# Performance work log

Measured on AMD Instinct MI355X. Metric: run time of the kernel, lower is better.

Reference implementation:

```python
import jax, jax.numpy as jnp
import numpy as np

T, B, D, H, O = 512, 256, 512, 256, 256
MLP_DIMS = [(D, 100), (100, 100), (100, 100), (100, 50), (50, H)]


def _linear_init(key, fan_in, fan_out):
    kw, kb = jax.random.split(key)
    lim = 1.0 / np.sqrt(fan_in)
    w = jax.random.uniform(kw, (fan_out, fan_in), minval=-lim, maxval=lim, dtype=jnp.float32)
    b = jax.random.uniform(kb, (fan_out,), minval=-lim, maxval=lim, dtype=jnp.float32)
    return w, b


def setup_inputs() -> dict:
    key = jax.random.key(0)
    ks = jax.random.split(key, 8)
    inp = {"x": jax.random.normal(ks[0], (T, B, D), dtype=jnp.float32)}
    for i, (fi, fo) in enumerate(MLP_DIMS):
        w, b = _linear_init(ks[1 + i], fi, fo)
        inp[f"wm{i + 1}"] = w
        inp[f"bm{i + 1}"] = b
    inp["wx"], inp["bx"] = _linear_init(ks[6], D, H)
    inp["wo"], inp["bo"] = _linear_init(ks[7], H, O)
    return inp


def reference(x, wm1, bm1, wm2, bm2, wm3, bm3, wm4, bm4, wm5, bm5, wx, bx, wo, bo):
    def step(h, xt):
        # xt: [B, D], h: [B, H]
        lx = xt @ wx.T + bx                      # linearX
        a = jax.nn.relu(xt @ wm1.T + bm1)        # layerMLP chain
        a = jax.nn.relu(a @ wm2.T + bm2)
        a = jax.nn.relu(a @ wm3.T + bm3)
        a = jax.nn.relu(a @ wm4.T + bm4)
        fx = jax.nn.sigmoid(a @ wm5.T + bm5)
        gate = fx * jax.nn.sigmoid(lx)
        h_new = jax.nn.relu(jnp.roll(h, 1, axis=-1) + gate)
        return h_new, None

    h0 = jnp.zeros((x.shape[1], wx.shape[0]), dtype=x.dtype)
    hidden, _ = jax.lax.scan(step, h0, x)
    output = hidden @ wo.T + bo                  # h2o
    return output, hidden
```

## Files before the change

kernel.cpp:

```cpp
#include <hip/hip_runtime.h>

typedef __attribute__((ext_vector_type(8))) short short8;
typedef __attribute__((ext_vector_type(4))) float f32x4;

#define OFF_WX 0
#define OFF_W1 131072
#define OFF_W2 196608
#define OFF_W3 212992
#define OFF_W4 229376
#define OFF_W5 237568
#define W_TOTAL 253952
#define TR 32

static __device__ __forceinline__ unsigned short f2bf(float f) {
    unsigned int u = __builtin_bit_cast(unsigned int, f);
    unsigned int r = (u + 0x7fffu + ((u >> 16) & 1u)) >> 16;
    return (unsigned short)r;
}
static __device__ __forceinline__ float bf2f(unsigned short h) {
    unsigned int u = ((unsigned int)h) << 16;
    return __builtin_bit_cast(float, u);
}
static __device__ __forceinline__ float sigmoidf(float z) {
    return 1.f / (1.f + __expf(-z));
}
static __device__ __forceinline__ void stA(unsigned short* dst, int r, int c, float v) {
    dst[(r << 7) + (((c >> 3) ^ (r & 7)) << 3) + (c & 7)] = f2bf(v);
}

__global__ __launch_bounds__(256) void prep_kernel(
    const float* __restrict__ wx, const float* __restrict__ wm1,
    const float* __restrict__ wm2, const float* __restrict__ wm3,
    const float* __restrict__ wm4, const float* __restrict__ wm5,
    unsigned short* __restrict__ wb, float* __restrict__ hid)
{
    const int stride = gridDim.x * blockDim.x;
    for (int idx = blockIdx.x * blockDim.x + threadIdx.x; idx < W_TOTAL; idx += stride) {
        float v;
        if (idx < OFF_W1) {
            v = wx[idx];
        } else if (idx < OFF_W2) {
            int j = idx - OFF_W1; int n = j >> 9, k = j & 511;
            v = (n < 100) ? wm1[n * 512 + k] : 0.f;
        } else if (idx < OFF_W3) {
            int j = idx - OFF_W2; int n = j >> 7, k = j & 127;
            v = (n < 100 && k < 100) ? wm2[n * 100 + k] : 0.f;
        } else if (idx < OFF_W4) {
            int j = idx - OFF_W3; int n = j >> 7, k = j & 127;
            v = (n < 100 && k < 100) ? wm3[n * 100 + k] : 0.f;
        } else if (idx < OFF_W5) {
            int j = idx - OFF_W4; int n = j >> 7, k = j & 127;
            v = (n < 50 && k < 100) ? wm4[n * 100 + k] : 0.f;
        } else {
            int j = idx - OFF_W5; int n = j >> 6, k = j & 63;
            v = (k < 50) ? wm5[n * 50 + k] : 0.f;
        }
        wb[idx] = f2bf(v);
    }
    for (int idx = blockIdx.x * blockDim.x + threadIdx.x; idx < 65536; idx += stride)
        hid[idx] = 0.f;
}

template<int KLOOP, int NI, typename Epi>
static __device__ __forceinline__ void stageS(const unsigned short* As,
                                              const unsigned short* __restrict__ Wg,
                                              int wave, int lane, Epi&& epi)
{
    f32x4 acc[NI][2];
#pragma unroll
    for (int i = 0; i < NI; i++) { acc[i][0] = {0,0,0,0}; acc[i][1] = {0,0,0,0}; }
    const int kp  = (lane >> 4) << 3;
    const int l15 = lane & 15;
#pragma unroll
    for (int k0 = 0; k0 < KLOOP; k0 += 32) {
        const int kb = (k0 >> 3) + (lane >> 4);
        short8 af[2];
#pragma unroll
        for (int mt = 0; mt < 2; mt++) {
            const int rm = mt * 16 + l15;
            af[mt] = *(const short8*)(As + (rm << 7) + ((kb ^ (rm & 7)) << 3));
        }
#pragma unroll
        for (int i = 0; i < NI; i++) {
            const int nt = wave + (i << 2);
            short8 bf = *(const short8*)(Wg + (nt * 16 + l15) * KLOOP + k0 + kp);
#pragma unroll
            for (int mt = 0; mt < 2; mt++)
                acc[i][mt] = __builtin_amdgcn_mfma_f32_16x16x32_bf16(
                    af[mt], bf, acc[i][mt], 0, 0, 0);
        }
    }
#pragma unroll
    for (int i = 0; i < NI; i++)
#pragma unroll
        for (int mt = 0; mt < 2; mt++)
            epi(i, wave + (i << 2), mt, acc[i][mt]);
}

__global__ __launch_bounds__(256, 4) void srnn_main(
    const float* __restrict__ x,
    const float* __restrict__ b1, const float* __restrict__ b2,
    const float* __restrict__ b3, const float* __restrict__ b4,
    const float* __restrict__ b5, const float* __restrict__ bx,
    const unsigned short* __restrict__ wb, float* __restrict__ hid)
{
    __shared__ __align__(16) unsigned short Xs[TR * 512];
    __shared__ __align__(16) unsigned short A1[TR * 128];
    unsigned short* A2 = Xs;
    unsigned short* Gs = Xs + 4096;

    const int tid  = threadIdx.x;
    const int wave = tid >> 6, lane = tid & 63;
    const int blk  = blockIdx.x;
    const int b    = blk >> 4;
    const int t0   = (blk & 15) << 5;
    const int l15  = lane & 15;
    const int rb   = (lane >> 4) << 2;
    const int kp   = (lane >> 4) << 3;

    {
        const int m0 = tid >> 7, c4 = tid & 127;
        const float* xbase = x + ((size_t)(t0 + m0) * 256 + b) * 512 + (c4 << 2);
        float4 xr[16];
#pragma unroll
        for (int it = 0; it < 16; it++)
            xr[it] = *(const float4*)(xbase + (size_t)it * 262144);
        const int blk8 = c4 >> 1, halfoff = (c4 & 1) << 2;
#pragma unroll
        for (int it = 0; it < 16; it++) {
            const int m = m0 + 2 * it;
            unsigned int p0 = (unsigned int)f2bf(xr[it].x) | ((unsigned int)f2bf(xr[it].y) << 16);
            unsigned int p1 = (unsigned int)f2bf(xr[it].z) | ((unsigned int)f2bf(xr[it].w) << 16);
            *(uint2*)&Xs[(m << 9) + ((blk8 ^ (m & 7)) << 3) + halfoff] = make_uint2(p0, p1);
        }
    }
    __syncthreads();

    f32x4 am1[2][2], alx[4][2];
#pragma unroll
    for (int i = 0; i < 2; i++) { am1[i][0] = {0,0,0,0}; am1[i][1] = {0,0,0,0}; }
#pragma unroll
    for (int i = 0; i < 4; i++) { alx[i][0] = {0,0,0,0}; alx[i][1] = {0,0,0,0}; }
    {
        const unsigned short* W1 = wb + OFF_W1;
        const unsigned short* WX = wb + OFF_WX;
#pragma unroll 4
        for (int k0 = 0; k0 < 512; k0 += 32) {
            const int kb = (k0 >> 3) + (lane >> 4);
            short8 af[2];
#pragma unroll
            for (int mt = 0; mt < 2; mt++) {
                const int rm = mt * 16 + l15;
                af[mt] = *(const short8*)(Xs + (rm << 9) + ((kb ^ (rm & 7)) << 3));
            }
#pragma unroll
            for (int i = 0; i < 2; i++) {
                short8 bf = *(const short8*)(W1 + ((wave + (i << 2)) * 16 + l15) * 512 + k0 + kp);
                am1[i][0] = __builtin_amdgcn_mfma_f32_16x16x32_bf16(af[0], bf, am1[i][0], 0, 0, 0);
                am1[i][1] = __builtin_amdgcn_mfma_f32_16x16x32_bf16(af[1], bf, am1[i][1], 0, 0, 0);
            }
#pragma unroll
            for (int i = 0; i < 4; i++) {
                short8 bf = *(const short8*)(WX + ((wave + (i << 2)) * 16 + l15) * 512 + k0 + kp);
                alx[i][0] = __builtin_amdgcn_mfma_f32_16x16x32_bf16(af[0], bf, alx[i][0], 0, 0, 0);
                alx[i][1] = __builtin_amdgcn_mfma_f32_16x16x32_bf16(af[1], bf, alx[i][1], 0, 0, 0);
            }
        }
#pragma unroll
        for (int i = 0; i < 2; i++) {
            const int c = (wave + (i << 2)) * 16 + l15;
            const float bb = (c < 100) ? b1[c] : 0.f;
#pragma unroll
            for (int mt = 0; mt < 2; mt++)
#pragma unroll
                for (int q = 0; q < 4; q++)
                    stA(A1, mt * 16 + rb + q, c,
                        (c < 100) ? fmaxf(am1[i][mt][q] + bb, 0.f) : 0.f);
        }
    }
    __syncthreads();

    stageS<128, 2>(A1, wb + OFF_W2, wave, lane, [&](int, int nt, int mt, f32x4 v) {
        const int c = nt * 16 + l15;
        const float bb = (c < 100) ? b2[c] : 0.f;
#pragma unroll
        for (int q = 0; q < 4; q++)
            stA(A2, mt * 16 + rb + q, c, (c < 100) ? fmaxf(v[q] + bb, 0.f) : 0.f);
    });
    __syncthreads();

    stageS<128, 2>(A2, wb + OFF_W3, wave, lane, [&](int, int nt, int mt, f32x4 v) {
        const int c = nt * 16 + l15;
        const float bb = (c < 100) ? b3[c] : 0.f;
#pragma unroll
        for (int q = 0; q < 4; q++)
            stA(A1, mt * 16 + rb + q, c, (c < 100) ? fmaxf(v[q] + bb, 0.f) : 0.f);
    });
    __syncthreads();

    stageS<128, 1>(A1, wb + OFF_W4, wave, lane, [&](int, int nt, int mt, f32x4 v) {
        const int c = nt * 16 + l15;
        const float bb = (c < 50) ? b4[c] : 0.f;
#pragma unroll
        for (int q = 0; q < 4; q++)
            stA(A2, mt * 16 + rb + q, c, (c < 50) ? fmaxf(v[q] + bb, 0.f) : 0.f);
    });
    __syncthreads();

    stageS<64, 4>(A2, wb + OFF_W5, wave, lane, [&](int i, int nt, int mt, f32x4 v) {
        const int c = nt * 16 + l15;
        const float bb5 = b5[c], bbx = bx[c];
#pragma unroll
        for (int q = 0; q < 4; q++) {
            const float g = sigmoidf(v[q] + bb5) * sigmoidf(alx[i][mt][q] + bbx);
            Gs[(mt * 16 + rb + q) * 256 + c] = f2bf(g);
        }
    });
    __syncthreads();

    {
        const int j = tid;
        const int base = (j + t0 + 1) & 255;
        float ph = 0.f;
#pragma unroll
        for (int m = 0; m < TR; m++)
            ph += bf2f(Gs[(m << 8) + ((base + m) & 255)]);
        atomicAdd(hid + b * 256 + j, ph);
    }
}

__global__ __launch_bounds__(256) void out_kernel(
    const float* __restrict__ hid, const float* __restrict__ wo,
    const float* __restrict__ bo, float* __restrict__ out)
{
    __shared__ __align__(16) float hrow[256];
    const int b = blockIdx.x, o = threadIdx.x;
    float h = hid[b * 256 + o];
    hrow[o] = h;
    out[65536 + b * 256 + o] = h;
    __syncthreads();
    const float4* wrow = (const float4*)(wo + o * 256);
    float s = bo[o];
#pragma unroll 8
    for (int k4 = 0; k4 < 64; k4++) {
        float4 w = wrow[k4];
        float4 hh = *(const float4*)&hrow[k4 * 4];
        s += hh.x * w.x + hh.y * w.y + hh.z * w.z + hh.w * w.w;
    }
    out[b * 256 + o] = s;
}

extern "C" void kernel_launch(void* const* d_in, const int* in_sizes, int n_in,
                              void* d_out, int out_size, void* d_ws, size_t ws_size,
                              hipStream_t stream)
{
    (void)in_sizes; (void)n_in; (void)out_size; (void)ws_size;
    const float* x   = (const float*)d_in[0];
    const float* wm1 = (const float*)d_in[1];
    const float* bm1 = (const float*)d_in[2];
    const float* wm2 = (const float*)d_in[3];
    const float* bm2 = (const float*)d_in[4];
    const float* wm3 = (const float*)d_in[5];
    const float* bm3 = (const float*)d_in[6];
    const float* wm4 = (const float*)d_in[7];
    const float* bm4 = (const float*)d_in[8];
    const float* wm5 = (const float*)d_in[9];
    const float* bm5 = (const float*)d_in[10];
    const float* wx  = (const float*)d_in[11];
    const float* bx  = (const float*)d_in[12];
    const float* wo  = (const float*)d_in[13];
    const float* bo  = (const float*)d_in[14];
    float* out = (float*)d_out;

    unsigned short* wb = (unsigned short*)d_ws;
    float* hid = (float*)((char*)d_ws + (size_t)W_TOTAL * 2);

    prep_kernel<<<512, 256, 0, stream>>>(wx, wm1, wm2, wm3, wm4, wm5, wb, hid);
    srnn_main<<<4096, 256, 0, stream>>>(x, bm1, bm2, bm3, bm4, bm5, bx, wb, hid);
    out_kernel<<<256, 256, 0, stream>>>(hid, wo, bo, out);
}
```

Before: 611.1 us.

## Use 512-thread blocks with per-wave N-tile split, wider swizzle, fused sigmoid gate

Doubles the main kernel's block size to 8 waves so that each wave owns fewer output tiles per stage. Stage 4 splits work across N and M tiles to keep all waves busy. The LDS XOR swizzle is widened from 8 to 16 row groups, and the gate buffer is also swizzled, to cut bank conflicts. The two sigmoids are fused into one reciprocal of a product of exponentials. This raises per-block parallelism and lowers register pressure, at the cost of more threads contending for the same shared memory and barriers.

Result: slower. 626.3 us (+2.5%).

```diff
diff --git a/kernel.cpp b/kernel.cpp
--- a/kernel.cpp
+++ b/kernel.cpp
@@ -21,12 +21,15 @@
     unsigned int u = ((unsigned int)h) << 16;
     return __builtin_bit_cast(float, u);
 }
-static __device__ __forceinline__ float sigmoidf(float z) {
-    return 1.f / (1.f + __expf(-z));
+static __device__ __forceinline__ float gate2(float a, float b) {
+    float ea = __expf(-a), eb = __expf(-b);
+    return __builtin_amdgcn_rcpf((1.f + ea) * (1.f + eb));
 }
 static __device__ __forceinline__ void stA(unsigned short* dst, int r, int c, float v) {
-    dst[(r << 7) + (((c >> 3) ^ (r & 7)) << 3) + (c & 7)] = f2bf(v);
-}
+    dst[(r << 7) + (((c >> 3) ^ (r & 15)) << 3) + (c & 7)] = f2bf(v);
+}
+
+#define MFMA(a, bfr, acc) __builtin_amdgcn_mfma_f32_16x16x32_bf16((a), (bfr), (acc), 0, 0, 0)
 
 __global__ __launch_bounds__(256) void prep_kernel(
     const float* __restrict__ wx, const float* __restrict__ wm1,
@@ -61,43 +64,7 @@
         hid[idx] = 0.f;
 }
 
-template<int KLOOP, int NI, typename Epi>
-static __device__ __forceinline__ void stageS(const unsigned short* As,
-                                              const unsigned short* __restrict__ Wg,
-                                              int wave, int lane, Epi&& epi)
-{
-    f32x4 acc[NI][2];
-#pragma unroll
-    for (int i = 0; i < NI; i++) { acc[i][0] = {0,0,0,0}; acc[i][1] = {0,0,0,0}; }
-    const int kp  = (lane >> 4) << 3;
-    const int l15 = lane & 15;
-#pragma unroll
-    for (int k0 = 0; k0 < KLOOP; k0 += 32) {
-        const int kb = (k0 >> 3) + (lane >> 4);
-        short8 af[2];
-#pragma unroll
-        for (int mt = 0; mt < 2; mt++) {
-            const int rm = mt * 16 + l15;
-            af[mt] = *(const short8*)(As + (rm << 7) + ((kb ^ (rm & 7)) << 3));
-        }
-#pragma unroll
-        for (int i = 0; i < NI; i++) {
-            const int nt = wave + (i << 2);
-            short8 bf = *(const short8*)(Wg + (nt * 16 + l15) * KLOOP + k0 + kp);
-#pragma unroll
-            for (int mt = 0; mt < 2; mt++)
-                acc[i][mt] = __builtin_amdgcn_mfma_f32_16x16x32_bf16(
-                    af[mt], bf, acc[i][mt], 0, 0, 0);
-        }
-    }
-#pragma unroll
-    for (int i = 0; i < NI; i++)
-#pragma unroll
-        for (int mt = 0; mt < 2; mt++)
-            epi(i, wave + (i << 2), mt, acc[i][mt]);
-}
-
-__global__ __launch_bounds__(256, 4) void srnn_main(
+__global__ __launch_bounds__(512, 8) void srnn_main(
     const float* __restrict__ x,
     const float* __restrict__ b1, const float* __restrict__ b2,
     const float* __restrict__ b3, const float* __restrict__ b4,
@@ -110,7 +77,7 @@
     unsigned short* Gs = Xs + 4096;
 
     const int tid  = threadIdx.x;
-    const int wave = tid >> 6, lane = tid & 63;
+    const int w    = tid >> 6, lane = tid & 63;
     const int blk  = blockIdx.x;
     const int b    = blk >> 4;
     const int t0   = (blk & 15) << 5;
@@ -119,112 +86,156 @@
     const int kp   = (lane >> 4) << 3;
 
     {
-        const int m0 = tid >> 7, c4 = tid & 127;
+        const int m0 = tid >> 7;
+        const int c4 = tid & 127;
         const float* xbase = x + ((size_t)(t0 + m0) * 256 + b) * 512 + (c4 << 2);
-        float4 xr[16];
-#pragma unroll
-        for (int it = 0; it < 16; it++)
-            xr[it] = *(const float4*)(xbase + (size_t)it * 262144);
+        float4 xr[8];
+#pragma unroll
+        for (int it = 0; it < 8; it++)
+            xr[it] = *(const float4*)(xbase + (size_t)it * 524288);
         const int blk8 = c4 >> 1, halfoff = (c4 & 1) << 2;
 #pragma unroll
-        for (int it = 0; it < 16; it++) {
-            const int m = m0 + 2 * it;
+        for (int it = 0; it < 8; it++) {
+            const int m = m0 + 4 * it;
             unsigned int p0 = (unsigned int)f2bf(xr[it].x) | ((unsigned int)f2bf(xr[it].y) << 16);
             unsigned int p1 = (unsigned int)f2bf(xr[it].z) | ((unsigned int)f2bf(xr[it].w) << 16);
-            *(uint2*)&Xs[(m << 9) + ((blk8 ^ (m & 7)) << 3) + halfoff] = make_uint2(p0, p1);
-        }
-    }
-    __syncthreads();
-
-    f32x4 am1[2][2], alx[4][2];
-#pragma unroll
-    for (int i = 0; i < 2; i++) { am1[i][0] = {0,0,0,0}; am1[i][1] = {0,0,0,0}; }
-#pragma unroll
-    for (int i = 0; i < 4; i++) { alx[i][0] = {0,0,0,0}; alx[i][1] = {0,0,0,0}; }
-    {
-        const unsigned short* W1 = wb + OFF_W1;
-        const unsigned short* WX = wb + OFF_WX;
+            *(uint2*)&Xs[(m << 9) + ((blk8 ^ (m & 15)) << 3) + halfoff] = make_uint2(p0, p1);
+        }
+    }
+    __syncthreads();
+
+    f32x4 am1[2], alx[2][2];
+    am1[0] = {0,0,0,0}; am1[1] = {0,0,0,0};
+#pragma unroll
+    for (int i = 0; i < 2; i++) { alx[i][0] = {0,0,0,0}; alx[i][1] = {0,0,0,0}; }
+    {
+        const unsigned short* W1r  = wb + OFF_W1 + (w * 16 + l15) * 512 + kp;
+        const unsigned short* WXr0 = wb + OFF_WX + (w * 16 + l15) * 512 + kp;
+        const unsigned short* WXr1 = wb + OFF_WX + ((w + 8) * 16 + l15) * 512 + kp;
 #pragma unroll 4
         for (int k0 = 0; k0 < 512; k0 += 32) {
             const int kb = (k0 >> 3) + (lane >> 4);
-            short8 af[2];
-#pragma unroll
-            for (int mt = 0; mt < 2; mt++) {
-                const int rm = mt * 16 + l15;
-                af[mt] = *(const short8*)(Xs + (rm << 9) + ((kb ^ (rm & 7)) << 3));
-            }
-#pragma unroll
-            for (int i = 0; i < 2; i++) {
-                short8 bf = *(const short8*)(W1 + ((wave + (i << 2)) * 16 + l15) * 512 + k0 + kp);
-                am1[i][0] = __builtin_amdgcn_mfma_f32_16x16x32_bf16(af[0], bf, am1[i][0], 0, 0, 0);
-                am1[i][1] = __builtin_amdgcn_mfma_f32_16x16x32_bf16(af[1], bf, am1[i][1], 0, 0, 0);
-            }
-#pragma unroll
-            for (int i = 0; i < 4; i++) {
-                short8 bf = *(const short8*)(WX + ((wave + (i << 2)) * 16 + l15) * 512 + k0 + kp);
-                alx[i][0] = __builtin_amdgcn_mfma_f32_16x16x32_bf16(af[0], bf, alx[i][0], 0, 0, 0);
-                alx[i][1] = __builtin_amdgcn_mfma_f32_16x16x32_bf16(af[1], bf, alx[i][1], 0, 0, 0);
-            }
+            const int xo = (kb ^ l15) << 3;
+            short8 af0 = *(const short8*)(Xs + (l15 << 9) + xo);
+            short8 af1 = *(const short8*)(Xs + ((16 + l15) << 9) + xo);
+            short8 b0  = *(const short8*)(W1r + k0);
+            short8 bx0 = *(const short8*)(WXr0 + k0);
+            short8 bx1 = *(const short8*)(WXr1 + k0);
+            am1[0]    = MFMA(af0, b0,  am1[0]);
+            am1[1]    = MFMA(af1, b0,  am1[1]);
+            alx[0][0] = MFMA(af0, bx0, alx[0][0]);
+            alx[0][1] = MFMA(af1, bx0, alx[0][1]);
+            alx[1][0] = MFMA(af0, bx1, alx[1][0]);
+            alx[1][1] = MFMA(af1, bx1, alx[1][1]);
+        }
+        const int c = w * 16 + l15;
+        const bool ok = (c < 100);
+        const float bb = ok ? b1[c] : 0.f;
+#pragma unroll
+        for (int mt = 0; mt < 2; mt++)
+#pragma unroll
+            for (int q = 0; q < 4; q++)
+                stA(A1, mt * 16 + rb + q, c, ok ? fmaxf(am1[mt][q] + bb, 0.f) : 0.f);
+    }
+    __syncthreads();
+
+    auto stage23 = [&](const unsigned short* As, const unsigned short* Wg,
+                       const float* __restrict__ bias, unsigned short* Ad) {
+        f32x4 acc[2];
+        acc[0] = {0,0,0,0}; acc[1] = {0,0,0,0};
+        const unsigned short* Wr = Wg + (w * 16 + l15) * 128 + kp;
+#pragma unroll
+        for (int k0 = 0; k0 < 128; k0 += 32) {
+            const int kb = (k0 >> 3) + (lane >> 4);
+            const int xo = (kb ^ l15) << 3;
+            short8 af0 = *(const short8*)(As + (l15 << 7) + xo);
+            short8 af1 = *(const short8*)(As + ((16 + l15) << 7) + xo);
+            short8 bf  = *(const short8*)(Wr + k0);
+            acc[0] = MFMA(af0, bf, acc[0]);
+            acc[1] = MFMA(af1, bf, acc[1]);
+        }
+        const int c = w * 16 + l15;
+        const bool ok = (c < 100);
+        const float bb = ok ? bias[c] : 0.f;
+#pragma unroll
+        for (int mt = 0; mt < 2; mt++)
+#pragma unroll
+            for (int q = 0; q < 4; q++)
+                stA(Ad, mt * 16 + rb + q, c, ok ? fmaxf(acc[mt][q] + bb, 0.f) : 0.f);
+    };
+    stage23(A1, wb + OFF_W2, b2, A2);
+    __syncthreads();
+    stage23(A2, wb + OFF_W3, b3, A1);
+    __syncthreads();
+
+    {
+        const int nt = w >> 1, mtl = w & 1;
+        f32x4 acc = {0,0,0,0};
+        const unsigned short* Wr = wb + OFF_W4 + (nt * 16 + l15) * 128 + kp;
+        const int rbase = mtl * 16 + l15;
+        const int rxo = rbase & 15;
+#pragma unroll
+        for (int k0 = 0; k0 < 128; k0 += 32) {
+            const int kb = (k0 >> 3) + (lane >> 4);
+            short8 af = *(const short8*)(A1 + (rbase << 7) + ((kb ^ rxo) << 3));
+            short8 bf = *(const short8*)(Wr + k0);
+            acc = MFMA(af, bf, acc);
+        }
+        const int c = nt * 16 + l15;
+        const bool ok = (c < 50);
+        const float bb = ok ? b4[c] : 0.f;
+#pragma unroll
+        for (int q = 0; q < 4; q++)
+            stA(A2, mtl * 16 + rb + q, c, ok ? fmaxf(acc[q] + bb, 0.f) : 0.f);
+    }
+    __syncthreads();
+
+    {
+        f32x4 a5[2][2];
+#pragma unroll
+        for (int i = 0; i < 2; i++) { a5[i][0] = {0,0,0,0}; a5[i][1] = {0,0,0,0}; }
+        const unsigned short* W5r0 = wb + OFF_W5 + (w * 16 + l15) * 64 + kp;
+        const unsigned short* W5r1 = wb + OFF_W5 + ((w + 8) * 16 + l15) * 64 + kp;
+#pragma unroll
+        for (int k0 = 0; k0 < 64; k0 += 32) {
+            const int kb = (k0 >> 3) + (lane >> 4);
+            const int xo = (kb ^ l15) << 3;
+            short8 af0 = *(const short8*)(A2 + (l15 << 7) + xo);
+            short8 af1 = *(const short8*)(A2 + ((16 + l15) << 7) + xo);
+            short8 bf0 = *(const short8*)(W5r0 + k0);
+            short8 bf1 = *(const short8*)(W5r1 + k0);
+            a5[0][0] = MFMA(af0, bf0, a5[0][0]);
+            a5[0][1] = MFMA(af1, bf0, a5[0][1]);
+            a5[1][0] = MFMA(af0, bf1, a5[1][0]);
+            a5[1][1] = MFMA(af1, bf1, a5[1][1]);
         }
 #pragma unroll
         for (int i = 0; i < 2; i++) {
-            const int c = (wave + (i << 2)) * 16 + l15;
-            const float bb = (c < 100) ? b1[c] : 0.f;
+            const int c = (w + 8 * i) * 16 + l15;
+            const float bb5 = b5[c], bbx = bx[c];
 #pragma unroll
             for (int mt = 0; mt < 2; mt++)
 #pragma unroll
-                for (int q = 0; q < 4; q++)
-                    stA(A1, mt * 16 + rb + q, c,
-                        (c < 100) ? fmaxf(am1[i][mt][q] + bb, 0.f) : 0.f);
-        }
-    }
-    __syncthreads();
-
-    stageS<128, 2>(A1, wb + OFF_W2, wave, lane, [&](int, int nt, int mt, f32x4 v) {
-        const int c = nt * 16 + l15;
-        const float bb = (c < 100) ? b2[c] : 0.f;
-#pragma unroll
-        for (int q = 0; q < 4; q++)
-            stA(A2, mt * 16 + rb + q, c, (c < 100) ? fmaxf(v[q] + bb, 0.f) : 0.f);
-    });
-    __syncthreads();
-
-    stageS<128, 2>(A2, wb + OFF_W3, wave, lane, [&](int, int nt, int mt, f32x4 v) {
-        const int c = nt * 16 + l15;
-        const float bb = (c < 100) ? b3[c] : 0.f;
-#pragma unroll
-        for (int q = 0; q < 4; q++)
-            stA(A1, mt * 16 + rb + q, c, (c < 100) ? fmaxf(v[q] + bb, 0.f) : 0.f);
-    });
-    __syncthreads();
-
-    stageS<128, 1>(A1, wb + OFF_W4, wave, lane, [&](int, int nt, int mt, f32x4 v) {
-        const int c = nt * 16 + l15;
-        const float bb = (c < 50) ? b4[c] : 0.f;
-#pragma unroll
-        for (int q = 0; q < 4; q++)
-            stA(A2, mt * 16 + rb + q, c, (c < 50) ? fmaxf(v[q] + bb, 0.f) : 0.f);
-    });
-    __syncthreads();
-
-    stageS<64, 4>(A2, wb + OFF_W5, wave, lane, [&](int i, int nt, int mt, f32x4 v) {
-        const int c = nt * 16 + l15;
-        const float bb5 = b5[c], bbx = bx[c];
-#pragma unroll
-        for (int q = 0; q < 4; q++) {
-            const float g = sigmoidf(v[q] + bb5) * sigmoidf(alx[i][mt][q] + bbx);
-            Gs[(mt * 16 + rb + q) * 256 + c] = f2bf(g);
-        }
-    });
-    __syncthreads();
-
-    {
-        const int j = tid;
+                for (int q = 0; q < 4; q++) {
+                    const float g = gate2(a5[i][mt][q] + bb5, alx[i][mt][q] + bbx);
+                    const int r = mt * 16 + rb + q;
+                    Gs[(r << 8) + (((c >> 3) ^ (r & 15)) << 3) + (c & 7)] = f2bf(g);
+                }
+        }
+    }
+    __syncthreads();
+
+    {
+        const int j    = tid & 255;
+        const int half = tid >> 8;
         const int base = (j + t0 + 1) & 255;
         float ph = 0.f;
 #pragma unroll
-        for (int m = 0; m < TR; m++)
-            ph += bf2f(Gs[(m << 8) + ((base + m) & 255)]);
+        for (int mm = 0; mm < 16; mm++) {
+            const int m  = half * 16 + mm;
+            const int cm = (base + m) & 255;
+            ph += bf2f(Gs[(m << 8) + (((cm >> 3) ^ (m & 15)) << 3) + (cm & 7)]);
+        }
         atomicAdd(hid + b * 256 + j, ph);
     }
 }
@@ -276,6 +287,6 @@
     float* hid = (float*)((char*)d_ws + (size_t)W_TOTAL * 2);
 
     prep_kernel<<<512, 256, 0, stream>>>(wx, wm1, wm2, wm3, wm4, wm5, wb, hid);
-    srnn_main<<<4096, 256, 0, stream>>>(x, bm1, bm2, bm3, bm4, bm5, bx, wb, hid);
+    srnn_main<<<4096, 512, 0, stream>>>(x, bm1, bm2, bm3, bm4, bm5, bx, wb, hid);
     out_kernel<<<256, 256, 0, stream>>>(hid, wo, bo, out);
 }
```
